# Optimization experiments

Hardware: AMD Instinct MI355X
Metric: run time of the kernel (lower is better)

## Reference

```python
import jax, jax.numpy as jnp
import numpy as np

N = 2048
DIM = 1024
NH = 16
DK = DIM // NH  # 64

def setup_inputs() -> dict:
    key = jax.random.key(0)
    kx, kq, kk, kv = jax.random.split(key, 4)
    # nn.Linear(dim_in, dim_in, bias=False): init ~ U(-1/sqrt(dim_in), 1/sqrt(dim_in))
    b = 1.0 / np.sqrt(DIM)
    return {
        "x": jax.random.normal(kx, (N, DIM), dtype=jnp.float32),
        "rela": jnp.zeros((1,), dtype=jnp.float32),  # unused by the module
        "Wq": jax.random.uniform(kq, (DIM, DIM), jnp.float32, -b, b),
        "Wk": jax.random.uniform(kk, (DIM, DIM), jnp.float32, -b, b),
        "Wv": jax.random.uniform(kv, (DIM, DIM), jnp.float32, -b, b),
    }

def reference(x, rela, Wq, Wk, Wv):
    n = x.shape[0]
    scale = 1.0 / np.sqrt(DK)
    # torch Linear: x @ W.T ; reshape to [n, nh, dk] then heads first -> [nh, n, dk]
    q = (x @ Wq.T).reshape(n, NH, DK).transpose(1, 0, 2)
    k = (x @ Wk.T).reshape(n, NH, DK).transpose(1, 0, 2)
    v = (x @ Wv.T).reshape(n, NH, DK).transpose(1, 0, 2)
    dist = jnp.einsum('hnd,hmd->hnm', q, k) * scale  # [nh, n, n]
    dist = jax.nn.softmax(dist, axis=-1)
    att = jnp.einsum('hnm,hmd->hnd', dist, v)        # [nh, n, dk]
    return att.transpose(1, 0, 2).reshape(n, DIM)
```

## Files before the change

kernel.cpp:

```cpp
#include <hip/hip_runtime.h>

#define SN 2048
#define SDIM 1024
#define SNH 16
#define SDK 64

typedef short short8 __attribute__((ext_vector_type(8)));
typedef short s16x4 __attribute__((ext_vector_type(4)));
typedef unsigned short u16;
typedef u16 u16x4 __attribute__((ext_vector_type(4)));
typedef float f32x4 __attribute__((ext_vector_type(4)));

__device__ __forceinline__ u16 f2b(float f){
  unsigned u = __builtin_bit_cast(unsigned, f);
  u += 0x7fffu + ((u >> 16) & 1u);
  return (u16)(u >> 16);
}

__device__ __forceinline__ float b2f(u16 b){
  unsigned u = ((unsigned)b) << 16;
  return __builtin_bit_cast(float, u);
}

__device__ __forceinline__ float fast_exp2(float x){
#if __has_builtin(__builtin_amdgcn_exp2f)
  return __builtin_amdgcn_exp2f(x);
#else
  float r; asm("v_exp_f32 %0, %1" : "=v"(r) : "v"(x)); return r;
#endif
}

__device__ __forceinline__ f32x4 mfma16(s16x4 a, s16x4 b, f32x4 c){
#if __has_builtin(__builtin_amdgcn_mfma_f32_16x16x16_bf16)
  return __builtin_amdgcn_mfma_f32_16x16x16_bf16(a, b, c, 0, 0, 0);
#elif __has_builtin(__builtin_amdgcn_mfma_f32_16x16x16bf16_1k)
  return __builtin_amdgcn_mfma_f32_16x16x16bf16_1k(a, b, c, 0, 0, 0);
#else
  asm volatile("v_mfma_f32_16x16x16_bf16 %0, %1, %2, %0" : "+v"(c) : "v"(a), "v"(b));
  return c;
#endif
}

__device__ __forceinline__ void async_cp16(const void* g, void* l){
  __builtin_amdgcn_global_load_lds(
      (const __attribute__((address_space(1))) unsigned*)g,
      (__attribute__((address_space(3))) unsigned*)l, 16, 0, 0);
}

__global__ void conv_all(const float* __restrict__ x, const float* __restrict__ wq,
                         const float* __restrict__ wk, const float* __restrict__ wv,
                         u16* __restrict__ xb, u16* __restrict__ wb){
  const int NX4 = (SN * SDIM) / 4;
  const int NW4 = (SDIM * SDIM) / 4;
  const int total = NX4 + 3 * NW4;
  int i = blockIdx.x * blockDim.x + threadIdx.x;
  int stride = gridDim.x * blockDim.x;
  for (int idx = i; idx < total; idx += stride){
    const float* src; u16* dst; int off;
    if (idx < NX4){ src = x; dst = xb; off = idx; }
    else {
      int t = idx - NX4; int ws = t >> 18; off = t & (NW4 - 1);
      src = (ws == 0) ? wq : ((ws == 1) ? wk : wv);
      dst = wb + (size_t)ws * SDIM * SDIM;
    }
    float4 v = reinterpret_cast<const float4*>(src)[off];
    u16x4 o = { f2b(v.x), f2b(v.y), f2b(v.z), f2b(v.w) };
    *reinterpret_cast<u16x4*>(&dst[(size_t)off * 4]) = o;
  }
}

__global__ __launch_bounds__(512) void proj_gemm(const u16* __restrict__ xb, const u16* __restrict__ wb,
                                                 u16* __restrict__ qb, u16* __restrict__ kb,
                                                 u16* __restrict__ vtb){
  __shared__ __align__(16) u16 Asm[2][64 * 64];
  __shared__ __align__(16) u16 Bsm[2][128 * 64];
  const int tid = threadIdx.x, w = tid >> 6, lane = tid & 63;
  const int r = lane & 15, hi = lane >> 4;
  const int tm = blockIdx.x * 64, tn = blockIdx.y * 128;
  const int z = blockIdx.z;
  const u16* W = wb + (size_t)z * SDIM * SDIM;
  const int wr = w >> 2, wc = w & 3;
  const int srow = lane >> 3;
  const int schunk = (lane & 7) ^ (lane >> 3);
  f32x4 acc[2][2] = {};

  auto stage = [&](int b, int kt){
    async_cp16(xb + (size_t)(tm + w * 8 + srow) * SDIM + kt + schunk * 8, &Asm[b][w * 8 * 64]);
#pragma unroll
    for (int c = 0; c < 2; c++){
      int row = w * 16 + c * 8;
      async_cp16(W + (size_t)(tn + row + srow) * SDIM + kt + schunk * 8, &Bsm[b][row * 64]);
    }
  };

  stage(0, 0);
  asm volatile("s_waitcnt vmcnt(0)" ::: "memory");
  __builtin_amdgcn_s_barrier();
  __builtin_amdgcn_sched_barrier(0);

  int cur = 0;
  for (int kt = 0; kt < SDIM; kt += 64){
    if (kt + 64 < SDIM) stage(cur ^ 1, kt + 64);
    __builtin_amdgcn_s_setprio(1);
#pragma unroll
    for (int kk = 0; kk < 2; kk++){
      short8 af[2], bf[2];
      int cc = (kk * 4 + hi) ^ (r & 7);
#pragma unroll
      for (int mr = 0; mr < 2; mr++)
        af[mr] = *reinterpret_cast<const short8*>(&Asm[cur][(wr * 32 + mr * 16 + r) * 64 + cc * 8]);
#pragma unroll
      for (int nr = 0; nr < 2; nr++)
        bf[nr] = *reinterpret_cast<const short8*>(&Bsm[cur][(wc * 32 + nr * 16 + r) * 64 + cc * 8]);
#pragma unroll
      for (int mr = 0; mr < 2; mr++)
#pragma unroll
        for (int nr = 0; nr < 2; nr++)
          acc[mr][nr] = __builtin_amdgcn_mfma_f32_16x16x32_bf16(af[mr], bf[nr], acc[mr][nr], 0, 0, 0);
    }
    __builtin_amdgcn_s_setprio(0);
    asm volatile("s_waitcnt vmcnt(0)" ::: "memory");
    __builtin_amdgcn_s_barrier();
    __builtin_amdgcn_sched_barrier(0);
    cur ^= 1;
  }

  if (z == 2){
#pragma unroll
    for (int mr = 0; mr < 2; mr++)
#pragma unroll
      for (int nr = 0; nr < 2; nr++){
        u16x4 o4 = { f2b(acc[mr][nr][0]), f2b(acc[mr][nr][1]),
                     f2b(acc[mr][nr][2]), f2b(acc[mr][nr][3]) };
        int col = tn + wc * 32 + nr * 16 + r;
        int row = tm + wr * 32 + mr * 16 + hi * 4;
        *reinterpret_cast<u16x4*>(&vtb[(size_t)col * SN + row]) = o4;
      }
  } else {
    u16* outp = (z == 0) ? qb : kb;
    const float scl = (z == 0) ? 0.18033688011112043f : 1.0f;
#pragma unroll
    for (int mr = 0; mr < 2; mr++)
#pragma unroll
      for (int nr = 0; nr < 2; nr++)
#pragma unroll
        for (int j = 0; j < 4; j++){
          int row = tm + wr * 32 + mr * 16 + hi * 4 + j;
          int col = tn + wc * 32 + nr * 16 + r;
          outp[(size_t)row * SDIM + col] = f2b(acc[mr][nr][j] * scl);
        }
  }
}

__global__ __launch_bounds__(256, 4) void attn(const u16* __restrict__ qb, const u16* __restrict__ kb,
                                               const u16* __restrict__ vtb,
                                               u16* __restrict__ po, float* __restrict__ pl){
  __shared__ __align__(16) u16 klds[2][64 * 64];
  __shared__ __align__(16) u16 vlds[2][64 * 64];
  const int tid = threadIdx.x, w = tid >> 6, lane = tid & 63;
  const int r = lane & 15, hi = lane >> 4;

  int flat = blockIdx.x + 16 * blockIdx.y + 256 * blockIdx.z;
  int sw = (flat & 7) * 128 + (flat >> 3);
  const int q0 = (sw & 15) * 128, h = (sw >> 4) & 15, z = sw >> 8;

  const int srow_off = lane >> 3;
  const int schunk   = (lane & 7) ^ (lane >> 3);

  short8 aq[2][2];
#pragma unroll
  for (int sub = 0; sub < 2; sub++){
    int qrow = q0 + w * 32 + sub * 16 + r;
    aq[sub][0] = *reinterpret_cast<const short8*>(&qb[(size_t)qrow * SDIM + h * SDK + hi * 8]);
    aq[sub][1] = *reinterpret_cast<const short8*>(&qb[(size_t)qrow * SDIM + h * SDK + 32 + hi * 8]);
  }
  f32x4 oacc[2][4] = {};
  float lacc0 = 0.f, lacc1 = 0.f;

  auto stage = [&](int b, int t){
#pragma unroll
    for (int c = 0; c < 2; c++){
      int row = w * 16 + c * 8 + srow_off;
      async_cp16(kb  + (size_t)(t + row) * SDIM + h * SDK + schunk * 8,
                 &klds[b][(w * 16 + c * 8) * 64]);
      async_cp16(vtb + (size_t)(h * SDK + row) * SN + t + schunk * 8,
                 &vlds[b][(w * 16 + c * 8) * 64]);
    }
  };

  const int t0 = z * (SN / 4), tend = t0 + (SN / 4);
  stage(0, t0);
  asm volatile("s_waitcnt vmcnt(0)" ::: "memory");
  __builtin_amdgcn_s_barrier();
  __builtin_amdgcn_sched_barrier(0);

  int cur = 0;
  for (int t = t0; t < tend; t += 64){
    if (t + 64 < tend) stage(cur ^ 1, t + 64);

    const u16* kbuf = &klds[cur][0];
    const u16* vbuf = &vlds[cur][0];

    f32x4 s0[4], s1[4];
    __builtin_amdgcn_s_setprio(1);
#pragma unroll
    for (int ct = 0; ct < 4; ct++){
      int row = ct * 16 + r;
      int c0 = hi ^ (r & 7);
      short8 bk0 = *reinterpret_cast<const short8*>(&kbuf[row * 64 + c0 * 8]);
      short8 bk1 = *reinterpret_cast<const short8*>(&kbuf[row * 64 + (c0 ^ 4) * 8]);
      f32x4 zero = {};
      s0[ct] = __builtin_amdgcn_mfma_f32_16x16x32_bf16(bk0, aq[0][0], zero, 0, 0, 0);
      s1[ct] = __builtin_amdgcn_mfma_f32_16x16x32_bf16(bk0, aq[1][0], zero, 0, 0, 0);
      s0[ct] = __builtin_amdgcn_mfma_f32_16x16x32_bf16(bk1, aq[0][1], s0[ct], 0, 0, 0);
      s1[ct] = __builtin_amdgcn_mfma_f32_16x16x32_bf16(bk1, aq[1][1], s1[ct], 0, 0, 0);
    }
    __builtin_amdgcn_s_setprio(0);

    s16x4 pa0[4], pa1[4];
#pragma unroll
    for (int ct = 0; ct < 4; ct++){
      float a0 = fast_exp2(s0[ct][0]), a1 = fast_exp2(s0[ct][1]);
      float a2 = fast_exp2(s0[ct][2]), a3 = fast_exp2(s0[ct][3]);
      lacc0 += (a0 + a1) + (a2 + a3);
      unsigned d0 = (__builtin_bit_cast(unsigned, a0) >> 16) |
                    (__builtin_bit_cast(unsigned, a1) & 0xffff0000u);
      unsigned d1 = (__builtin_bit_cast(unsigned, a2) >> 16) |
                    (__builtin_bit_cast(unsigned, a3) & 0xffff0000u);
      uint2 dd0 = { d0, d1 };
      pa0[ct] = __builtin_bit_cast(s16x4, dd0);
      float b0 = fast_exp2(s1[ct][0]), b1 = fast_exp2(s1[ct][1]);
      float b2 = fast_exp2(s1[ct][2]), b3 = fast_exp2(s1[ct][3]);
      lacc1 += (b0 + b1) + (b2 + b3);
      unsigned e0 = (__builtin_bit_cast(unsigned, b0) >> 16) |
                    (__builtin_bit_cast(unsigned, b1) & 0xffff0000u);
      unsigned e1 = (__builtin_bit_cast(unsigned, b2) >> 16) |
                    (__builtin_bit_cast(unsigned, b3) & 0xffff0000u);
      uint2 dd1 = { e0, e1 };
      pa1[ct] = __builtin_bit_cast(s16x4, dd1);
    }

    __builtin_amdgcn_s_setprio(1);
#pragma unroll
    for (int dt = 0; dt < 4; dt++){
      int row = dt * 16 + r;
      int swz = row & 7;
      s16x4 bvd[4];
#pragma unroll
      for (int ct = 0; ct < 4; ct++){
        int chunk = (2 * ct + (hi >> 1)) ^ swz;
        bvd[ct] = *reinterpret_cast<const s16x4*>(&vbuf[row * 64 + chunk * 8 + (hi & 1) * 4]);
      }
#pragma unroll
      for (int ct = 0; ct < 4; ct++){
        oacc[0][dt] = mfma16(pa0[ct], bvd[ct], oacc[0][dt]);
        oacc[1][dt] = mfma16(pa1[ct], bvd[ct], oacc[1][dt]);
      }
    }
    __builtin_amdgcn_s_setprio(0);

    asm volatile("s_waitcnt vmcnt(0)" ::: "memory");
    __builtin_amdgcn_s_barrier();
    __builtin_amdgcn_sched_barrier(0);
    cur ^= 1;
  }

  lacc0 += __shfl_xor(lacc0, 16); lacc0 += __shfl_xor(lacc0, 32);
  lacc1 += __shfl_xor(lacc1, 16); lacc1 += __shfl_xor(lacc1, 32);

  const size_t zh = (size_t)z * SNH + h;
#pragma unroll
  for (int sub = 0; sub < 2; sub++)
#pragma unroll
    for (int dt = 0; dt < 4; dt++)
#pragma unroll
      for (int j = 0; j < 4; j++){
        int row = q0 + w * 32 + sub * 16 + hi * 4 + j;
        po[(zh * SN + row) * SDK + dt * 16 + r] = f2b(oacc[sub][dt][j]);
      }
  if (hi == 0){
    pl[zh * SN + q0 + w * 32 + r] = lacc0;
    pl[zh * SN + q0 + w * 32 + 16 + r] = lacc1;
  }
}

__global__ void merge(const u16* __restrict__ po, const float* __restrict__ pl,
                      float* __restrict__ out){
  int gid = blockIdx.x * blockDim.x + threadIdx.x;
  int c4 = gid & 15;
  int rowid = gid >> 4;
  int h = rowid & 15, q = rowid >> 4;
  float L = 0.f;
  float4 o = { 0.f, 0.f, 0.f, 0.f };
#pragma unroll
  for (int z = 0; z < 4; z++){
    size_t zh = (size_t)z * SNH + h;
    L += pl[zh * SN + q];
    u16x4 a = *reinterpret_cast<const u16x4*>(&po[(zh * SN + q) * SDK + c4 * 4]);
    o.x += b2f(a[0]); o.y += b2f(a[1]); o.z += b2f(a[2]); o.w += b2f(a[3]);
  }
  float rL = 1.0f / L;
  o.x *= rL; o.y *= rL; o.z *= rL; o.w *= rL;
  reinterpret_cast<float4*>(&out[(size_t)q * SDIM + h * SDK])[c4] = o;
}

extern "C" void kernel_launch(void* const* d_in, const int* in_sizes, int n_in,
                              void* d_out, int out_size, void* d_ws, size_t ws_size,
                              hipStream_t stream){
  const float* x  = (const float*)d_in[0];
  const float* Wq = (const float*)d_in[2];
  const float* Wk = (const float*)d_in[3];
  const float* Wv = (const float*)d_in[4];
  float* out = (float*)d_out;

  char* ws = (char*)d_ws;
  u16* xb  = (u16*)(ws);
  u16* wb  = (u16*)(ws + (4  << 20));
  u16* qb  = (u16*)(ws + (10 << 20));
  u16* kb  = (u16*)(ws + (14 << 20));
  u16* vtb = (u16*)(ws + (18 << 20));
  u16* po  = (u16*)(ws + (22 << 20));
  float* pl = (float*)(ws + (38 << 20));

  conv_all<<<2048, 256, 0, stream>>>(x, Wq, Wk, Wv, xb, wb);

  dim3 pg(SN / 64, SDIM / 128, 3);
  proj_gemm<<<pg, 512, 0, stream>>>(xb, wb, qb, kb, vtb);

  dim3 ag(SN / 128, SNH, 4);
  attn<<<ag, 256, 0, stream>>>(qb, kb, vtb, po, pl);

  merge<<<(SN * SNH * 16) / 256, 256, 0, stream>>>(po, pl, out);
}
```

Before: 60.78 us.

## Use 16x16x32 MFMA for PV via K-row permutation and enlarge projection GEMM tiles

```diff
diff --git a/kernel.cpp b/kernel.cpp
--- a/kernel.cpp
+++ b/kernel.cpp
@@ -9,6 +9,7 @@
 typedef short s16x4 __attribute__((ext_vector_type(4)));
 typedef unsigned short u16;
 typedef u16 u16x4 __attribute__((ext_vector_type(4)));
+typedef unsigned u32x4 __attribute__((ext_vector_type(4)));
 typedef float f32x4 __attribute__((ext_vector_type(4)));
 
 __device__ __forceinline__ u16 f2b(float f){
@@ -27,17 +28,6 @@
   return __builtin_amdgcn_exp2f(x);
 #else
   float r; asm("v_exp_f32 %0, %1" : "=v"(r) : "v"(x)); return r;
-#endif
-}
-
-__device__ __forceinline__ f32x4 mfma16(s16x4 a, s16x4 b, f32x4 c){
-#if __has_builtin(__builtin_amdgcn_mfma_f32_16x16x16_bf16)
-  return __builtin_amdgcn_mfma_f32_16x16x16_bf16(a, b, c, 0, 0, 0);
-#elif __has_builtin(__builtin_amdgcn_mfma_f32_16x16x16bf16_1k)
-  return __builtin_amdgcn_mfma_f32_16x16x16bf16_1k(a, b, c, 0, 0, 0);
-#else
-  asm volatile("v_mfma_f32_16x16x16_bf16 %0, %1, %2, %0" : "+v"(c) : "v"(a), "v"(b));
-  return c;
 #endif
 }
 
@@ -69,27 +59,33 @@
   }
 }
 
-__global__ __launch_bounds__(512) void proj_gemm(const u16* __restrict__ xb, const u16* __restrict__ wb,
+__global__ __launch_bounds__(256) void proj_gemm(const u16* __restrict__ xb, const u16* __restrict__ wb,
                                                  u16* __restrict__ qb, u16* __restrict__ kb,
                                                  u16* __restrict__ vtb){
-  __shared__ __align__(16) u16 Asm[2][64 * 64];
+  __shared__ __align__(16) u16 Asm[2][128 * 64];
   __shared__ __align__(16) u16 Bsm[2][128 * 64];
   const int tid = threadIdx.x, w = tid >> 6, lane = tid & 63;
   const int r = lane & 15, hi = lane >> 4;
-  const int tm = blockIdx.x * 64, tn = blockIdx.y * 128;
-  const int z = blockIdx.z;
+
+  int flat = blockIdx.x + 16 * blockIdx.y + 128 * blockIdx.z;
+  int sw = (flat & 7) * 48 + (flat >> 3);
+  const int tm = (sw & 15) * 128;
+  int rest = sw >> 4;
+  const int tn = (rest & 7) * 128;
+  const int z = rest >> 3;
+
   const u16* W = wb + (size_t)z * SDIM * SDIM;
-  const int wr = w >> 2, wc = w & 3;
+  const int wr = w >> 1, wc = w & 1;
   const int srow = lane >> 3;
   const int schunk = (lane & 7) ^ (lane >> 3);
-  f32x4 acc[2][2] = {};
+  f32x4 acc[4][4] = {};
 
   auto stage = [&](int b, int kt){
-    async_cp16(xb + (size_t)(tm + w * 8 + srow) * SDIM + kt + schunk * 8, &Asm[b][w * 8 * 64]);
-#pragma unroll
-    for (int c = 0; c < 2; c++){
-      int row = w * 16 + c * 8;
-      async_cp16(W + (size_t)(tn + row + srow) * SDIM + kt + schunk * 8, &Bsm[b][row * 64]);
+#pragma unroll
+    for (int c = 0; c < 4; c++){
+      int row = w * 32 + c * 8;
+      async_cp16(xb + (size_t)(tm + row + srow) * SDIM + kt + schunk * 8, &Asm[b][row * 64]);
+      async_cp16(W  + (size_t)(tn + row + srow) * SDIM + kt + schunk * 8, &Bsm[b][row * 64]);
     }
   };
 
@@ -104,18 +100,18 @@
     __builtin_amdgcn_s_setprio(1);
 #pragma unroll
     for (int kk = 0; kk < 2; kk++){
-      short8 af[2], bf[2];
+      short8 af[4], bf[4];
       int cc = (kk * 4 + hi) ^ (r & 7);
 #pragma unroll
-      for (int mr = 0; mr < 2; mr++)
-        af[mr] = *reinterpret_cast<const short8*>(&Asm[cur][(wr * 32 + mr * 16 + r) * 64 + cc * 8]);
-#pragma unroll
-      for (int nr = 0; nr < 2; nr++)
-        bf[nr] = *reinterpret_cast<const short8*>(&Bsm[cur][(wc * 32 + nr * 16 + r) * 64 + cc * 8]);
-#pragma unroll
-      for (int mr = 0; mr < 2; mr++)
-#pragma unroll
-        for (int nr = 0; nr < 2; nr++)
+      for (int mr = 0; mr < 4; mr++)
+        af[mr] = *reinterpret_cast<const short8*>(&Asm[cur][(wr * 64 + mr * 16 + r) * 64 + cc * 8]);
+#pragma unroll
+      for (int nr = 0; nr < 4; nr++)
+        bf[nr] = *reinterpret_cast<const short8*>(&Bsm[cur][(wc * 64 + nr * 16 + r) * 64 + cc * 8]);
+#pragma unroll
+      for (int mr = 0; mr < 4; mr++)
+#pragma unroll
+        for (int nr = 0; nr < 4; nr++)
           acc[mr][nr] = __builtin_amdgcn_mfma_f32_16x16x32_bf16(af[mr], bf[nr], acc[mr][nr], 0, 0, 0);
     }
     __builtin_amdgcn_s_setprio(0);
@@ -127,32 +123,32 @@
 
   if (z == 2){
 #pragma unroll
-    for (int mr = 0; mr < 2; mr++)
-#pragma unroll
-      for (int nr = 0; nr < 2; nr++){
+    for (int mr = 0; mr < 4; mr++)
+#pragma unroll
+      for (int nr = 0; nr < 4; nr++){
         u16x4 o4 = { f2b(acc[mr][nr][0]), f2b(acc[mr][nr][1]),
                      f2b(acc[mr][nr][2]), f2b(acc[mr][nr][3]) };
-        int col = tn + wc * 32 + nr * 16 + r;
-        int row = tm + wr * 32 + mr * 16 + hi * 4;
+        int col = tn + wc * 64 + nr * 16 + r;
+        int row = tm + wr * 64 + mr * 16 + hi * 4;
         *reinterpret_cast<u16x4*>(&vtb[(size_t)col * SN + row]) = o4;
       }
   } else {
     u16* outp = (z == 0) ? qb : kb;
     const float scl = (z == 0) ? 0.18033688011112043f : 1.0f;
 #pragma unroll
-    for (int mr = 0; mr < 2; mr++)
-#pragma unroll
-      for (int nr = 0; nr < 2; nr++)
+    for (int mr = 0; mr < 4; mr++)
+#pragma unroll
+      for (int nr = 0; nr < 4; nr++)
 #pragma unroll
         for (int j = 0; j < 4; j++){
-          int row = tm + wr * 32 + mr * 16 + hi * 4 + j;
-          int col = tn + wc * 32 + nr * 16 + r;
+          int row = tm + wr * 64 + mr * 16 + hi * 4 + j;
+          int col = tn + wc * 64 + nr * 16 + r;
           outp[(size_t)row * SDIM + col] = f2b(acc[mr][nr][j] * scl);
         }
   }
 }
 
-__global__ __launch_bounds__(256, 4) void attn(const u16* __restrict__ qb, const u16* __restrict__ kb,
+__global__ __launch_bounds__(256, 3) void attn(const u16* __restrict__ qb, const u16* __restrict__ kb,
                                                const u16* __restrict__ vtb,
                                                u16* __restrict__ po, float* __restrict__ pl){
   __shared__ __align__(16) u16 klds[2][64 * 64];
@@ -180,9 +176,11 @@
   auto stage = [&](int b, int t){
 #pragma unroll
     for (int c = 0; c < 2; c++){
-      int row = w * 16 + c * 8 + srow_off;
-      async_cp16(kb  + (size_t)(t + row) * SDIM + h * SDK + schunk * 8,
+      int rho = w * 16 + c * 8 + srow_off;
+      int kvp = 32 * (rho >> 5) + 8 * ((rho >> 2) & 3) + 4 * ((rho >> 4) & 1) + (rho & 3);
+      async_cp16(kb  + (size_t)(t + kvp) * SDIM + h * SDK + schunk * 8,
                  &klds[b][(w * 16 + c * 8) * 64]);
+      int row = rho;
       async_cp16(vtb + (size_t)(h * SDK + row) * SN + t + schunk * 8,
                  &vlds[b][(w * 16 + c * 8) * 64]);
     }
@@ -217,27 +215,31 @@
     }
     __builtin_amdgcn_s_setprio(0);
 
-    s16x4 pa0[4], pa1[4];
+    uint2 pc0[4], pc1[4];
 #pragma unroll
     for (int ct = 0; ct < 4; ct++){
       float a0 = fast_exp2(s0[ct][0]), a1 = fast_exp2(s0[ct][1]);
       float a2 = fast_exp2(s0[ct][2]), a3 = fast_exp2(s0[ct][3]);
       lacc0 += (a0 + a1) + (a2 + a3);
-      unsigned d0 = (__builtin_bit_cast(unsigned, a0) >> 16) |
-                    (__builtin_bit_cast(unsigned, a1) & 0xffff0000u);
-      unsigned d1 = (__builtin_bit_cast(unsigned, a2) >> 16) |
-                    (__builtin_bit_cast(unsigned, a3) & 0xffff0000u);
-      uint2 dd0 = { d0, d1 };
-      pa0[ct] = __builtin_bit_cast(s16x4, dd0);
+      pc0[ct].x = (__builtin_bit_cast(unsigned, a0) >> 16) |
+                  (__builtin_bit_cast(unsigned, a1) & 0xffff0000u);
+      pc0[ct].y = (__builtin_bit_cast(unsigned, a2) >> 16) |
+                  (__builtin_bit_cast(unsigned, a3) & 0xffff0000u);
       float b0 = fast_exp2(s1[ct][0]), b1 = fast_exp2(s1[ct][1]);
       float b2 = fast_exp2(s1[ct][2]), b3 = fast_exp2(s1[ct][3]);
       lacc1 += (b0 + b1) + (b2 + b3);
-      unsigned e0 = (__builtin_bit_cast(unsigned, b0) >> 16) |
-                    (__builtin_bit_cast(unsigned, b1) & 0xffff0000u);
-      unsigned e1 = (__builtin_bit_cast(unsigned, b2) >> 16) |
-                    (__builtin_bit_cast(unsigned, b3) & 0xffff0000u);
-      uint2 dd1 = { e0, e1 };
-      pa1[ct] = __builtin_bit_cast(s16x4, dd1);
+      pc1[ct].x = (__builtin_bit_cast(unsigned, b0) >> 16) |
+                  (__builtin_bit_cast(unsigned, b1) & 0xffff0000u);
+      pc1[ct].y = (__builtin_bit_cast(unsigned, b2) >> 16) |
+                  (__builtin_bit_cast(unsigned, b3) & 0xffff0000u);
+    }
+    short8 paf0[2], paf1[2];
+#pragma unroll
+    for (int c = 0; c < 2; c++){
+      u32x4 u0 = { pc0[2*c].x, pc0[2*c].y, pc0[2*c+1].x, pc0[2*c+1].y };
+      u32x4 u1 = { pc1[2*c].x, pc1[2*c].y, pc1[2*c+1].x, pc1[2*c+1].y };
+      paf0[c] = __builtin_bit_cast(short8, u0);
+      paf1[c] = __builtin_bit_cast(short8, u1);
     }
 
     __builtin_amdgcn_s_setprio(1);
@@ -245,16 +247,14 @@
     for (int dt = 0; dt < 4; dt++){
       int row = dt * 16 + r;
       int swz = row & 7;
-      s16x4 bvd[4];
-#pragma unroll
-      for (int ct = 0; ct < 4; ct++){
-        int chunk = (2 * ct + (hi >> 1)) ^ swz;
-        bvd[ct] = *reinterpret_cast<const s16x4*>(&vbuf[row * 64 + chunk * 8 + (hi & 1) * 4]);
-      }
-#pragma unroll
-      for (int ct = 0; ct < 4; ct++){
-        oacc[0][dt] = mfma16(pa0[ct], bvd[ct], oacc[0][dt]);
-        oacc[1][dt] = mfma16(pa1[ct], bvd[ct], oacc[1][dt]);
+      short8 bvc[2];
+#pragma unroll
+      for (int c = 0; c < 2; c++)
+        bvc[c] = *reinterpret_cast<const short8*>(&vbuf[row * 64 + ((4 * c + hi) ^ swz) * 8]);
+#pragma unroll
+      for (int c = 0; c < 2; c++){
+        oacc[0][dt] = __builtin_amdgcn_mfma_f32_16x16x32_bf16(paf0[c], bvc[c], oacc[0][dt], 0, 0, 0);
+        oacc[1][dt] = __builtin_amdgcn_mfma_f32_16x16x32_bf16(paf1[c], bvc[c], oacc[1][dt], 0, 0, 0);
       }
     }
     __builtin_amdgcn_s_setprio(0);
@@ -324,8 +324,8 @@
 
   conv_all<<<2048, 256, 0, stream>>>(x, Wq, Wk, Wv, xb, wb);
 
-  dim3 pg(SN / 64, SDIM / 128, 3);
-  proj_gemm<<<pg, 512, 0, stream>>>(xb, wb, qb, kb, vtb);
+  dim3 pg(SDIM / 64, SDIM / 128, 3);
+  proj_gemm<<<pg, 256, 0, stream>>>(xb, wb, qb, kb, vtb);
 
   dim3 ag(SN / 128, SNH, 4);
   attn<<<ag, 256, 0, stream>>>(qb, kb, vtb, po, pl);
```

Result: slower. 64.42 us (+6.0%).
